# Optimization experiments

Measured on AMD Instinct MI355X. Metric: run time of the kernel, lower is better.

The kernel has to match this reference:

```python
import jax, jax.numpy as jnp
import numpy as np

R = 4          # self.radius
NS = 256       # self.out_num_samples


def conv2d(x, w, b=None, padding=1, dilation=1):
    out = jax.lax.conv_general_dilated(
        x, w, window_strides=(1, 1),
        padding=[(padding, padding), (padding, padding)],
        rhs_dilation=(dilation, dilation),
        dimension_numbers=('NCHW', 'OIHW', 'NCHW'))
    if b is not None:
        out = out + b[None, :, None, None]
    return out


def depth_regression(logits):
    # softmax over 256 depth hypotheses, then expectation over a 9-wide
    # window centered at the argmax (clamped to [0, NS-1]).
    prob = jax.nn.softmax(logits, axis=1)                      # [B,256,H,W]
    amax = jnp.argmax(prob, axis=1, keepdims=True)             # [B,1,H,W] int
    offs = jnp.arange(-R, R + 1).reshape(1, 2 * R + 1, 1, 1)
    idx = jnp.clip(amax + offs, 0, NS - 1)                     # [B,9,H,W]
    p = jnp.take_along_axis(prob, idx, axis=1)                 # [B,9,H,W]
    num = jnp.sum(idx.astype(prob.dtype) * p, axis=1, keepdims=True)
    den = 1e-6 + jnp.sum(p, axis=1, keepdims=True)
    nd = (num / den) / (NS - 1.0)                              # [B,1,H,W]
    return nd, prob


def setup_inputs() -> dict:
    key = jax.random.key(0)
    ks = jax.random.split(key, 16)
    B, H, W = 4, 256, 320
    HD = 32            # hidden_dim
    CD = 32            # corr channels; input_dim = CD + 1 = 33
    CIN = HD + 1 + CD  # 65, GRU conv input channels

    def w(k, shape):
        fan = int(np.prod(shape[1:]))
        return (jax.random.normal(k, shape, jnp.float32) / np.sqrt(fan)).astype(jnp.float32)

    return {
        'hidden': jnp.tanh(jax.random.normal(ks[0], (B, HD, H, W), jnp.float32)),
        'normalized_depth': jax.random.uniform(ks[1], (B, 1, H, W), dtype=jnp.float32),
        'corr': jax.random.normal(ks[2], (B, CD, H, W), jnp.float32),
        # ConvGRU params (3x3, padding 1, with bias)
        'convz_w': w(ks[3], (HD, CIN, 3, 3)), 'convz_b': jnp.zeros((HD,), jnp.float32),
        'convr_w': w(ks[4], (HD, CIN, 3, 3)), 'convr_b': jnp.zeros((HD,), jnp.float32),
        'convq_w': w(ks[5], (HD, CIN, 3, 3)), 'convq_b': jnp.zeros((HD,), jnp.float32),
        # depth_head: 3x3 dil2 (no bias) -> 1x1 (no bias) -> 1x1 (bias)
        'dh1_w': w(ks[6], (32, HD, 3, 3)),
        'dh2_w': w(ks[7], (64, 32, 1, 1)),
        'dh3_w': w(ks[8], (NS, 64, 1, 1)), 'dh3_b': jnp.zeros((NS,), jnp.float32),
        # confidence_head: 3x3 dil2 (no bias) -> 1x1 (bias)
        'ch1_w': w(ks[9], (32, HD, 3, 3)),
        'ch2_w': w(ks[10], (1, 32, 1, 1)), 'ch2_b': jnp.zeros((1,), jnp.float32),
    }


def reference(hidden, normalized_depth, corr,
              convz_w, convz_b, convr_w, convr_b, convq_w, convq_b,
              dh1_w, dh2_w, dh3_w, dh3_b, ch1_w, ch2_w, ch2_b):
    # cat = [normalized_depth, corr]
    x = jnp.concatenate([normalized_depth, corr], axis=1)      # [B,33,H,W]
    # ConvGRU (confidence=None branch)
    hx = jnp.concatenate([hidden, x], axis=1)                  # [B,65,H,W]
    z = jax.nn.sigmoid(conv2d(hx, convz_w, convz_b))
    r = jax.nn.sigmoid(conv2d(hx, convr_w, convr_b))
    q = jnp.tanh(conv2d(jnp.concatenate([r * hidden, x], axis=1), convq_w, convq_b))
    h = (1.0 - z) * hidden + z * q                             # [B,32,H,W]
    # confidence head (confidence_flag=True)
    conf0 = conv2d(jax.nn.relu(conv2d(h, ch1_w, padding=2, dilation=2)),
                   ch2_w, ch2_b, padding=0)                    # [B,1,H,W]
    conf = jax.nn.sigmoid(conf0)
    # depth head
    t = jax.nn.relu(conv2d(h, dh1_w, padding=2, dilation=2))
    t = jax.nn.relu(conv2d(t, dh2_w, padding=0))
    logits = conv2d(t, dh3_w, dh3_b, padding=0)                # [B,256,H,W]
    nd, prob = depth_regression(logits)
    return h, nd, prob, conf, conf0
```

## Files before the change

kernel.cpp:

```cpp
#include <hip/hip_runtime.h>

#define WDT 320
#define HGT 256
#define HWSZ 81920
#define NPIX 327680

__device__ __forceinline__ float sigm(float x){ return 1.0f/(1.0f + __expf(-x)); }
__device__ __forceinline__ float tanh_(float x){
  float e = __expf(-2.0f*fabsf(x));
  float t = (1.0f - e)/(1.0f + e);
  return x < 0.0f ? -t : t;
}

__global__ __launch_bounds__(256) void k_wprep(
    const float* __restrict__ zw, const float* __restrict__ rw,
    const float* __restrict__ qw, const float* __restrict__ d1w,
    const float* __restrict__ c1w, const float* __restrict__ d2w,
    const float* __restrict__ d3w,
    float* __restrict__ W1, float* __restrict__ W2, float* __restrict__ W3,
    float* __restrict__ Wd2, float* __restrict__ Wd3)
{
  const int N1 = 9*65*64, N2 = 9*65*32, N3 = 9*32*64, N4 = 32*64, N5 = 64*256;
  int i = blockIdx.x*256 + threadIdx.x;
  if (i < N1){
    int tc = i >> 6, co = i & 63;
    int tap = tc / 65, cin = tc % 65;
    float v = (co < 32) ? zw[(size_t)(co*65 + cin)*9 + tap]
                        : rw[(size_t)((co-32)*65 + cin)*9 + tap];
    W1[i] = v;
  } else if (i < N1 + N2){
    int j = i - N1;
    int tc = j >> 5, co = j & 31;
    int tap = tc / 65, cin = tc % 65;
    W2[j] = qw[(size_t)(co*65 + cin)*9 + tap];
  } else if (i < N1 + N2 + N3){
    int j = i - (N1 + N2);
    int tc = j >> 6, co = j & 63;
    int tap = tc >> 5, cin = tc & 31;
    float v = (co < 32) ? d1w[(size_t)(co*32 + cin)*9 + tap]
                        : c1w[(size_t)((co-32)*32 + cin)*9 + tap];
    W3[j] = v;
  } else if (i < N1 + N2 + N3 + N4){
    int j = i - (N1 + N2 + N3);
    int cin = j >> 6, co = j & 63;
    Wd2[j] = d2w[co*32 + cin];
  } else if (i < N1 + N2 + N3 + N4 + N5){
    int j = i - (N1 + N2 + N3 + N4);
    int cin = j >> 8, co = j & 255;
    Wd3[j] = d3w[co*64 + cin];
  }
}

__global__ __launch_bounds__(256) void k_gru1(
    const float* __restrict__ hidden, const float* __restrict__ ndp,
    const float* __restrict__ corr, const float* __restrict__ W1,
    const float* __restrict__ zb, const float* __restrict__ rb,
    float* __restrict__ zpl, float* __restrict__ rhpl)
{
  int p = blockIdx.x*256 + threadIdx.x;
  int row = p / WDT;
  int x = p - row*WDT;
  int yimg = row & (HGT-1);
  int b = row >> 8;
  size_t hbase = (size_t)b*32*HWSZ + (size_t)(p - b*HWSZ);
  float acc[64];
  #pragma unroll
  for (int i=0;i<64;++i) acc[i]=0.f;
  #pragma unroll
  for (int ty=0; ty<3; ++ty){
    int dy = ty-1;
    if ((unsigned)(yimg+dy) >= (unsigned)HGT) continue;
    #pragma unroll
    for (int tx=0; tx<3; ++tx){
      int dx = tx-1;
      bool okx = (unsigned)(x+dx) < (unsigned)WDT;
      int off = dy*WDT + dx;
      const float* wt = W1 + (ty*3+tx)*65*64;
      #pragma unroll 1
      for (int c=0;c<32;++c){
        float v = okx ? hidden[hbase + (size_t)c*HWSZ + off] : 0.f;
        const float* w = wt + c*64;
        #pragma unroll
        for (int i=0;i<64;++i) acc[i] = fmaf(w[i], v, acc[i]);
      }
      {
        float v = okx ? ndp[p + off] : 0.f;
        const float* w = wt + 32*64;
        #pragma unroll
        for (int i=0;i<64;++i) acc[i] = fmaf(w[i], v, acc[i]);
      }
      #pragma unroll 1
      for (int c=0;c<32;++c){
        float v = okx ? corr[hbase + (size_t)c*HWSZ + off] : 0.f;
        const float* w = wt + (33+c)*64;
        #pragma unroll
        for (int i=0;i<64;++i) acc[i] = fmaf(w[i], v, acc[i]);
      }
    }
  }
  #pragma unroll
  for (int c=0;c<32;++c)
    zpl[(size_t)c*NPIX + p] = sigm(acc[c] + zb[c]);
  #pragma unroll
  for (int c=0;c<32;++c){
    float r = sigm(acc[32+c] + rb[c]);
    rhpl[(size_t)c*NPIX + p] = r * hidden[hbase + (size_t)c*HWSZ];
  }
}

__global__ __launch_bounds__(256) void k_gru2(
    const float* __restrict__ hidden, const float* __restrict__ ndp,
    const float* __restrict__ corr, const float* __restrict__ rhpl,
    const float* __restrict__ zpl, const float* __restrict__ W2,
    const float* __restrict__ qb, float* __restrict__ out_h)
{
  int p = blockIdx.x*256 + threadIdx.x;
  int row = p / WDT;
  int x = p - row*WDT;
  int yimg = row & (HGT-1);
  int b = row >> 8;
  size_t hbase = (size_t)b*32*HWSZ + (size_t)(p - b*HWSZ);
  float acc[32];
  #pragma unroll
  for (int i=0;i<32;++i) acc[i]=0.f;
  #pragma unroll
  for (int ty=0; ty<3; ++ty){
    int dy = ty-1;
    if ((unsigned)(yimg+dy) >= (unsigned)HGT) continue;
    #pragma unroll
    for (int tx=0; tx<3; ++tx){
      int dx = tx-1;
      bool okx = (unsigned)(x+dx) < (unsigned)WDT;
      int off = dy*WDT + dx;
      const float* wt = W2 + (ty*3+tx)*65*32;
      #pragma unroll 1
      for (int c=0;c<32;++c){
        float v = okx ? rhpl[(size_t)c*NPIX + p + off] : 0.f;
        const float* w = wt + c*32;
        #pragma unroll
        for (int i=0;i<32;++i) acc[i] = fmaf(w[i], v, acc[i]);
      }
      {
        float v = okx ? ndp[p + off] : 0.f;
        const float* w = wt + 32*32;
        #pragma unroll
        for (int i=0;i<32;++i) acc[i] = fmaf(w[i], v, acc[i]);
      }
      #pragma unroll 1
      for (int c=0;c<32;++c){
        float v = okx ? corr[hbase + (size_t)c*HWSZ + off] : 0.f;
        const float* w = wt + (33+c)*32;
        #pragma unroll
        for (int i=0;i<32;++i) acc[i] = fmaf(w[i], v, acc[i]);
      }
    }
  }
  #pragma unroll
  for (int c=0;c<32;++c){
    float qv = tanh_(acc[c] + qb[c]);
    float z  = zpl[(size_t)c*NPIX + p];
    float h0 = hidden[hbase + (size_t)c*HWSZ];
    out_h[hbase + (size_t)c*HWSZ] = (1.0f - z)*h0 + z*qv;
  }
}

__global__ __launch_bounds__(256) void k_heads(
    const float* __restrict__ out_h, const float* __restrict__ W3,
    const float* __restrict__ c2w, const float* __restrict__ c2b,
    float* __restrict__ t1pl, float* __restrict__ out_conf, float* __restrict__ out_conf0)
{
  int p = blockIdx.x*256 + threadIdx.x;
  int row = p / WDT;
  int x = p - row*WDT;
  int yimg = row & (HGT-1);
  int b = row >> 8;
  size_t hbase = (size_t)b*32*HWSZ + (size_t)(p - b*HWSZ);
  float acc[64];
  #pragma unroll
  for (int i=0;i<64;++i) acc[i]=0.f;
  #pragma unroll
  for (int ty=0; ty<3; ++ty){
    int dy = (ty-1)*2;
    if ((unsigned)(yimg+dy) >= (unsigned)HGT) continue;
    #pragma unroll
    for (int tx=0; tx<3; ++tx){
      int dx = (tx-1)*2;
      bool okx = (unsigned)(x+dx) < (unsigned)WDT;
      int off = dy*WDT + dx;
      const float* wt = W3 + (ty*3+tx)*32*64;
      #pragma unroll 1
      for (int c=0;c<32;++c){
        float v = okx ? out_h[hbase + (size_t)c*HWSZ + off] : 0.f;
        const float* w = wt + c*64;
        #pragma unroll
        for (int i=0;i<64;++i) acc[i] = fmaf(w[i], v, acc[i]);
      }
    }
  }
  #pragma unroll
  for (int c=0;c<32;++c)
    t1pl[(size_t)c*NPIX + p] = fmaxf(acc[c], 0.f);
  float conf0 = c2b[0];
  #pragma unroll
  for (int i=0;i<32;++i)
    conf0 = fmaf(fmaxf(acc[32+i], 0.f), c2w[i], conf0);
  out_conf0[p] = conf0;
  out_conf[p]  = sigm(conf0);
}

__global__ __launch_bounds__(256) void k_depth(
    const float* __restrict__ t1pl, const float* __restrict__ Wd2,
    const float* __restrict__ Wd3, const float* __restrict__ d3b,
    float* __restrict__ out_prob, float* __restrict__ out_nd)
{
  __shared__ float t2l[64][65];
  __shared__ float redA[4][64];
  __shared__ int   redI[4][64];
  __shared__ float redB[4][64];
  __shared__ float redC[4][64];
  int tid = threadIdx.x, lane = tid & 63;
  int wvu = __builtin_amdgcn_readfirstlane(tid >> 6);
  int p = blockIdx.x*64 + lane;
  float a1[16];
  #pragma unroll
  for (int i=0;i<16;++i) a1[i]=0.f;
  const float* Wd2b = Wd2 + wvu*16;
  #pragma unroll 2
  for (int c=0;c<32;++c){
    float v = t1pl[(size_t)c*NPIX + p];
    const float* w = Wd2b + c*64;
    #pragma unroll
    for (int i=0;i<16;++i) a1[i] = fmaf(w[i], v, a1[i]);
  }
  #pragma unroll
  for (int i=0;i<16;++i) t2l[lane][wvu*16+i] = fmaxf(a1[i], 0.f);
  __syncthreads();
  float acc[64];
  #pragma unroll
  for (int i=0;i<64;++i) acc[i]=0.f;
  const float* Wd3b = Wd3 + wvu*64;
  #pragma unroll 2
  for (int c=0;c<64;++c){
    float v = t2l[lane][c];
    const float* w = Wd3b + c*256;
    #pragma unroll
    for (int i=0;i<64;++i) acc[i] = fmaf(w[i], v, acc[i]);
  }
  const float* bb = d3b + wvu*64;
  float mx = -1e30f; int am = 0;
  #pragma unroll
  for (int i=0;i<64;++i){
    float l = acc[i] + bb[i];
    acc[i] = l;
    if (l > mx){ mx = l; am = wvu*64+i; }
  }
  redA[wvu][lane] = mx; redI[wvu][lane] = am;
  __syncthreads();
  float gmx = redA[0][lane]; int gam = redI[0][lane];
  #pragma unroll
  for (int w2=1; w2<4; ++w2){
    float m = redA[w2][lane]; int a = redI[w2][lane];
    if (m > gmx || (m == gmx && a < gam)){ gmx = m; gam = a; }
  }
  float s = 0.f;
  #pragma unroll
  for (int i=0;i<64;++i){
    float e = __expf(acc[i] - gmx);
    acc[i] = e; s += e;
  }
  redB[wvu][lane] = s;
  __syncthreads();
  float gs = redB[0][lane] + redB[1][lane] + redB[2][lane] + redB[3][lane];
  float inv = 1.0f / gs;
  int b = p / HWSZ;
  int qq = p - b*HWSZ;
  size_t obase = (size_t)b*256*HWSZ + qq;
  int lo = gam - 4, hi = gam + 4;
  float num = 0.f, den = 0.f;
  #pragma unroll
  for (int i=0;i<64;++i){
    int m = wvu*64 + i;
    float pr = acc[i] * inv;
    out_prob[obase + (size_t)m*HWSZ] = pr;
    int mlt = (m >= lo && m <= hi) ? 1 : 0;
    if (m == 0 && lo < 0) mlt = 1 - lo;
    if (m == 255 && hi > 255) mlt = hi - 254;
    num += (float)(m*mlt) * pr;
    den += (float)mlt * pr;
  }
  redA[wvu][lane] = num; redC[wvu][lane] = den;
  __syncthreads();
  if (wvu == 0){
    float tn = redA[0][lane]+redA[1][lane]+redA[2][lane]+redA[3][lane];
    float td = redC[0][lane]+redC[1][lane]+redC[2][lane]+redC[3][lane];
    out_nd[p] = (tn / (1e-6f + td)) * (1.0f/255.0f);
  }
}

extern "C" void kernel_launch(void* const* d_in, const int* in_sizes, int n_in,
                              void* d_out, int out_size, void* d_ws, size_t ws_size,
                              hipStream_t stream)
{
  const float* hidden = (const float*)d_in[0];
  const float* ndp    = (const float*)d_in[1];
  const float* corr   = (const float*)d_in[2];
  const float* zw  = (const float*)d_in[3];
  const float* zb  = (const float*)d_in[4];
  const float* rw  = (const float*)d_in[5];
  const float* rb  = (const float*)d_in[6];
  const float* qw  = (const float*)d_in[7];
  const float* qb  = (const float*)d_in[8];
  const float* d1w = (const float*)d_in[9];
  const float* d2w = (const float*)d_in[10];
  const float* d3w = (const float*)d_in[11];
  const float* d3b = (const float*)d_in[12];
  const float* c1w = (const float*)d_in[13];
  const float* c2w = (const float*)d_in[14];
  const float* c2b = (const float*)d_in[15];
  float* out = (float*)d_out;

  float* ws   = (float*)d_ws;
  float* zpl  = ws;
  float* rhpl = ws + 10485760;
  float* t1pl = ws + 20971520;
  float* W1   = ws + 31457280;
  float* W2   = W1 + 37440;
  float* W3   = W2 + 18720;
  float* Wd2  = W3 + 18432;
  float* Wd3  = Wd2 + 2048;

  float* out_h     = out;
  float* out_nd    = out + 10485760;
  float* out_prob  = out + 10813440;
  float* out_conf  = out + 94699520;
  float* out_conf0 = out + 95027200;

  k_wprep<<<364, 256, 0, stream>>>(zw, rw, qw, d1w, c1w, d2w, d3w, W1, W2, W3, Wd2, Wd3);
  k_gru1 <<<NPIX/256, 256, 0, stream>>>(hidden, ndp, corr, W1, zb, rb, zpl, rhpl);
  k_gru2 <<<NPIX/256, 256, 0, stream>>>(hidden, ndp, corr, rhpl, zpl, W2, qb, out_h);
  k_heads<<<NPIX/256, 256, 0, stream>>>(out_h, W3, c2w, c2b, t1pl, out_conf, out_conf0);
  k_depth<<<NPIX/64, 256, 0, stream>>>(t1pl, Wd2, Wd3, d3b, out_prob, out_nd);
}
```

Before: 1.255 ms.

## Stage conv input rows in shared memory with one block per image row

The three 3x3 conv kernels now give each block one full image row of 320 threads. Each input channel's three source rows are staged into a double-buffered shared-memory strip with zero-padded halo, so horizontal taps read LDS instead of issuing nine redundant global loads. The next channel is prefetched into registers while the current one is consumed, and block indices are swizzled across rows. The cost is a __syncthreads per channel, and the occupancy hint in launch bounds may cause register pressure or spills given the 64-float accumulators.

```diff
diff --git a/kernel.cpp b/kernel.cpp
--- a/kernel.cpp
+++ b/kernel.cpp
@@ -51,152 +51,184 @@
   }
 }
 
-__global__ __launch_bounds__(256) void k_gru1(
+
+__global__ __launch_bounds__(320, 5) void k_gru1(
     const float* __restrict__ hidden, const float* __restrict__ ndp,
     const float* __restrict__ corr, const float* __restrict__ W1,
     const float* __restrict__ zb, const float* __restrict__ rb,
     float* __restrict__ zpl, float* __restrict__ rhpl)
 {
-  int p = blockIdx.x*256 + threadIdx.x;
-  int row = p / WDT;
-  int x = p - row*WDT;
-  int yimg = row & (HGT-1);
-  int b = row >> 8;
-  size_t hbase = (size_t)b*32*HWSZ + (size_t)(p - b*HWSZ);
+  __shared__ float sm[2][3][322];
+  int bid = blockIdx.x;
+  int rowg = (bid & 7)*128 + (bid >> 3);
+  int yimg = rowg & (HGT-1);
+  int b = rowg >> 8;
+  int x = threadIdx.x;
+  if (x == 0){
+    #pragma unroll
+    for (int bb=0;bb<2;++bb)
+      #pragma unroll
+      for (int r=0;r<3;++r){ sm[bb][r][0]=0.f; sm[bb][r][321]=0.f; }
+  }
+  const float* hpl = hidden + (size_t)b*32*HWSZ + yimg*WDT + x;
+  const float* cpl = corr   + (size_t)b*32*HWSZ + yimg*WDT + x;
+  const float* npl = ndp    + (size_t)b*HWSZ   + yimg*WDT + x;
+
+  auto srcval = [&](int c, int r)->float {
+    int yy = yimg + (r-1);
+    if ((unsigned)yy >= (unsigned)HGT) return 0.f;
+    int doff = (r-1)*WDT;
+    if (c < 32)  return hpl[(size_t)c*HWSZ + doff];
+    if (c == 32) return npl[doff];
+    return cpl[(size_t)(c-33)*HWSZ + doff];
+  };
+
   float acc[64];
   #pragma unroll
   for (int i=0;i<64;++i) acc[i]=0.f;
-  #pragma unroll
-  for (int ty=0; ty<3; ++ty){
-    int dy = ty-1;
-    if ((unsigned)(yimg+dy) >= (unsigned)HGT) continue;
-    #pragma unroll
-    for (int tx=0; tx<3; ++tx){
-      int dx = tx-1;
-      bool okx = (unsigned)(x+dx) < (unsigned)WDT;
-      int off = dy*WDT + dx;
-      const float* wt = W1 + (ty*3+tx)*65*64;
-      #pragma unroll 1
-      for (int c=0;c<32;++c){
-        float v = okx ? hidden[hbase + (size_t)c*HWSZ + off] : 0.f;
-        const float* w = wt + c*64;
+  float v0 = srcval(0,0), v1 = srcval(0,1), v2 = srcval(0,2);
+  #pragma unroll 1
+  for (int c=0;c<65;++c){
+    int cur = c & 1;
+    sm[cur][0][x+1]=v0; sm[cur][1][x+1]=v1; sm[cur][2][x+1]=v2;
+    if (c < 64){ v0=srcval(c+1,0); v1=srcval(c+1,1); v2=srcval(c+1,2); }
+    __syncthreads();
+    const float* wc = W1 + c*64;
+    #pragma unroll
+    for (int ty=0;ty<3;++ty){
+      #pragma unroll
+      for (int tx=0;tx<3;++tx){
+        float vv = sm[cur][ty][x+tx];
+        const float* w = wc + (ty*3+tx)*65*64;
         #pragma unroll
-        for (int i=0;i<64;++i) acc[i] = fmaf(w[i], v, acc[i]);
-      }
-      {
-        float v = okx ? ndp[p + off] : 0.f;
-        const float* w = wt + 32*64;
-        #pragma unroll
-        for (int i=0;i<64;++i) acc[i] = fmaf(w[i], v, acc[i]);
-      }
-      #pragma unroll 1
-      for (int c=0;c<32;++c){
-        float v = okx ? corr[hbase + (size_t)c*HWSZ + off] : 0.f;
-        const float* w = wt + (33+c)*64;
-        #pragma unroll
-        for (int i=0;i<64;++i) acc[i] = fmaf(w[i], v, acc[i]);
+        for (int i=0;i<64;++i) acc[i] = fmaf(w[i], vv, acc[i]);
       }
     }
   }
+  int p = rowg*WDT + x;
   #pragma unroll
   for (int c=0;c<32;++c)
     zpl[(size_t)c*NPIX + p] = sigm(acc[c] + zb[c]);
   #pragma unroll
   for (int c=0;c<32;++c){
     float r = sigm(acc[32+c] + rb[c]);
-    rhpl[(size_t)c*NPIX + p] = r * hidden[hbase + (size_t)c*HWSZ];
-  }
-}
-
-__global__ __launch_bounds__(256) void k_gru2(
+    rhpl[(size_t)c*NPIX + p] = r * hpl[(size_t)c*HWSZ];
+  }
+}
+
+__global__ __launch_bounds__(320) void k_gru2(
     const float* __restrict__ hidden, const float* __restrict__ ndp,
     const float* __restrict__ corr, const float* __restrict__ rhpl,
     const float* __restrict__ zpl, const float* __restrict__ W2,
     const float* __restrict__ qb, float* __restrict__ out_h)
 {
-  int p = blockIdx.x*256 + threadIdx.x;
-  int row = p / WDT;
-  int x = p - row*WDT;
-  int yimg = row & (HGT-1);
-  int b = row >> 8;
-  size_t hbase = (size_t)b*32*HWSZ + (size_t)(p - b*HWSZ);
+  __shared__ float sm[2][3][322];
+  int bid = blockIdx.x;
+  int rowg = (bid & 7)*128 + (bid >> 3);
+  int yimg = rowg & (HGT-1);
+  int b = rowg >> 8;
+  int x = threadIdx.x;
+  if (x == 0){
+    #pragma unroll
+    for (int bb=0;bb<2;++bb)
+      #pragma unroll
+      for (int r=0;r<3;++r){ sm[bb][r][0]=0.f; sm[bb][r][321]=0.f; }
+  }
+  const float* rpl = rhpl + (size_t)b*HWSZ + yimg*WDT + x;
+  const float* cpl = corr + (size_t)b*32*HWSZ + yimg*WDT + x;
+  const float* npl = ndp  + (size_t)b*HWSZ   + yimg*WDT + x;
+  const float* hpl = hidden + (size_t)b*32*HWSZ + yimg*WDT + x;
+
+  auto srcval = [&](int c, int r)->float {
+    int yy = yimg + (r-1);
+    if ((unsigned)yy >= (unsigned)HGT) return 0.f;
+    int doff = (r-1)*WDT;
+    if (c < 32)  return rpl[(size_t)c*NPIX + doff];
+    if (c == 32) return npl[doff];
+    return cpl[(size_t)(c-33)*HWSZ + doff];
+  };
+
   float acc[32];
   #pragma unroll
   for (int i=0;i<32;++i) acc[i]=0.f;
-  #pragma unroll
-  for (int ty=0; ty<3; ++ty){
-    int dy = ty-1;
-    if ((unsigned)(yimg+dy) >= (unsigned)HGT) continue;
-    #pragma unroll
-    for (int tx=0; tx<3; ++tx){
-      int dx = tx-1;
-      bool okx = (unsigned)(x+dx) < (unsigned)WDT;
-      int off = dy*WDT + dx;
-      const float* wt = W2 + (ty*3+tx)*65*32;
-      #pragma unroll 1
-      for (int c=0;c<32;++c){
-        float v = okx ? rhpl[(size_t)c*NPIX + p + off] : 0.f;
-        const float* w = wt + c*32;
+  float v0 = srcval(0,0), v1 = srcval(0,1), v2 = srcval(0,2);
+  #pragma unroll 1
+  for (int c=0;c<65;++c){
+    int cur = c & 1;
+    sm[cur][0][x+1]=v0; sm[cur][1][x+1]=v1; sm[cur][2][x+1]=v2;
+    if (c < 64){ v0=srcval(c+1,0); v1=srcval(c+1,1); v2=srcval(c+1,2); }
+    __syncthreads();
+    const float* wc = W2 + c*32;
+    #pragma unroll
+    for (int ty=0;ty<3;++ty){
+      #pragma unroll
+      for (int tx=0;tx<3;++tx){
+        float vv = sm[cur][ty][x+tx];
+        const float* w = wc + (ty*3+tx)*65*32;
         #pragma unroll
-        for (int i=0;i<32;++i) acc[i] = fmaf(w[i], v, acc[i]);
-      }
-      {
-        float v = okx ? ndp[p + off] : 0.f;
-        const float* w = wt + 32*32;
-        #pragma unroll
-        for (int i=0;i<32;++i) acc[i] = fmaf(w[i], v, acc[i]);
-      }
-      #pragma unroll 1
-      for (int c=0;c<32;++c){
-        float v = okx ? corr[hbase + (size_t)c*HWSZ + off] : 0.f;
-        const float* w = wt + (33+c)*32;
-        #pragma unroll
-        for (int i=0;i<32;++i) acc[i] = fmaf(w[i], v, acc[i]);
+        for (int i=0;i<32;++i) acc[i] = fmaf(w[i], vv, acc[i]);
       }
     }
   }
+  int p = rowg*WDT + x;
   #pragma unroll
   for (int c=0;c<32;++c){
     float qv = tanh_(acc[c] + qb[c]);
     float z  = zpl[(size_t)c*NPIX + p];
-    float h0 = hidden[hbase + (size_t)c*HWSZ];
-    out_h[hbase + (size_t)c*HWSZ] = (1.0f - z)*h0 + z*qv;
-  }
-}
-
-__global__ __launch_bounds__(256) void k_heads(
+    float h0 = hpl[(size_t)c*HWSZ];
+    out_h[(size_t)b*32*HWSZ + (size_t)c*HWSZ + yimg*WDT + x] = (1.0f - z)*h0 + z*qv;
+  }
+}
+
+__global__ __launch_bounds__(320, 5) void k_heads(
     const float* __restrict__ out_h, const float* __restrict__ W3,
     const float* __restrict__ c2w, const float* __restrict__ c2b,
     float* __restrict__ t1pl, float* __restrict__ out_conf, float* __restrict__ out_conf0)
 {
-  int p = blockIdx.x*256 + threadIdx.x;
-  int row = p / WDT;
-  int x = p - row*WDT;
-  int yimg = row & (HGT-1);
-  int b = row >> 8;
-  size_t hbase = (size_t)b*32*HWSZ + (size_t)(p - b*HWSZ);
+  __shared__ float sm[2][3][324];
+  int bid = blockIdx.x;
+  int rowg = (bid & 7)*128 + (bid >> 3);
+  int yimg = rowg & (HGT-1);
+  int b = rowg >> 8;
+  int x = threadIdx.x;
+  if (x < 2){
+    #pragma unroll
+    for (int bb=0;bb<2;++bb)
+      #pragma unroll
+      for (int r=0;r<3;++r){ sm[bb][r][x]=0.f; sm[bb][r][322+x]=0.f; }
+  }
+  const float* hpl = out_h + (size_t)b*32*HWSZ + yimg*WDT + x;
+
+  auto srcval = [&](int c, int r)->float {
+    int yy = yimg + (r-1)*2;
+    if ((unsigned)yy >= (unsigned)HGT) return 0.f;
+    int doff = (r-1)*2*WDT;
+    return hpl[(size_t)c*HWSZ + doff];
+  };
+
   float acc[64];
   #pragma unroll
   for (int i=0;i<64;++i) acc[i]=0.f;
-  #pragma unroll
-  for (int ty=0; ty<3; ++ty){
-    int dy = (ty-1)*2;
-    if ((unsigned)(yimg+dy) >= (unsigned)HGT) continue;
-    #pragma unroll
-    for (int tx=0; tx<3; ++tx){
-      int dx = (tx-1)*2;
-      bool okx = (unsigned)(x+dx) < (unsigned)WDT;
-      int off = dy*WDT + dx;
-      const float* wt = W3 + (ty*3+tx)*32*64;
-      #pragma unroll 1
-      for (int c=0;c<32;++c){
-        float v = okx ? out_h[hbase + (size_t)c*HWSZ + off] : 0.f;
-        const float* w = wt + c*64;
+  float v0 = srcval(0,0), v1 = srcval(0,1), v2 = srcval(0,2);
+  #pragma unroll 1
+  for (int c=0;c<32;++c){
+    int cur = c & 1;
+    sm[cur][0][x+2]=v0; sm[cur][1][x+2]=v1; sm[cur][2][x+2]=v2;
+    if (c < 31){ v0=srcval(c+1,0); v1=srcval(c+1,1); v2=srcval(c+1,2); }
+    __syncthreads();
+    const float* wc = W3 + c*64;
+    #pragma unroll
+    for (int ty=0;ty<3;++ty){
+      #pragma unroll
+      for (int tx=0;tx<3;++tx){
+        float vv = sm[cur][ty][x + tx*2];
+        const float* w = wc + (ty*3+tx)*32*64;
         #pragma unroll
-        for (int i=0;i<64;++i) acc[i] = fmaf(w[i], v, acc[i]);
+        for (int i=0;i<64;++i) acc[i] = fmaf(w[i], vv, acc[i]);
       }
     }
   }
+  int p = rowg*WDT + x;
   #pragma unroll
   for (int c=0;c<32;++c)
     t1pl[(size_t)c*NPIX + p] = fmaxf(acc[c], 0.f);
@@ -336,8 +368,8 @@
   float* out_conf0 = out + 95027200;
 
   k_wprep<<<364, 256, 0, stream>>>(zw, rw, qw, d1w, c1w, d2w, d3w, W1, W2, W3, Wd2, Wd3);
-  k_gru1 <<<NPIX/256, 256, 0, stream>>>(hidden, ndp, corr, W1, zb, rb, zpl, rhpl);
-  k_gru2 <<<NPIX/256, 256, 0, stream>>>(hidden, ndp, corr, rhpl, zpl, W2, qb, out_h);
-  k_heads<<<NPIX/256, 256, 0, stream>>>(out_h, W3, c2w, c2b, t1pl, out_conf, out_conf0);
+  k_gru1 <<<1024, 320, 0, stream>>>(hidden, ndp, corr, W1, zb, rb, zpl, rhpl);
+  k_gru2 <<<1024, 320, 0, stream>>>(hidden, ndp, corr, rhpl, zpl, W2, qb, out_h);
+  k_heads<<<1024, 320, 0, stream>>>(out_h, W3, c2w, c2b, t1pl, out_conf, out_conf0);
   k_depth<<<NPIX/64, 256, 0, stream>>>(t1pl, Wd2, Wd3, d3b, out_prob, out_nd);
 }
```

Measured after the change: 2.137 ms. 1.7x slower.
